# Kernel tuning notes

Hardware: AMD Instinct MI355X
Metric: run time of the kernel (lower is better)

Reference implementation:

```python
import jax, jax.numpy as jnp
import numpy as np

C = 256
RED = 8
DQK = C // RED  # 32


def setup_inputs() -> dict:
    key = jax.random.key(0)
    ks = jax.random.split(key, 8)
    B, H, W = 8, 64, 64
    x = jax.random.normal(ks[0], (B, C, H, W), dtype=jnp.float32)
    # 1x1 conv weights stored as [out, in]; biases [out]
    Wq = jax.random.normal(ks[1], (DQK, C), dtype=jnp.float32) * 0.02
    bq = jax.random.normal(ks[2], (DQK,), dtype=jnp.float32) * 0.02
    Wk = jax.random.normal(ks[3], (DQK, C), dtype=jnp.float32) * 0.02
    bk = jax.random.normal(ks[4], (DQK,), dtype=jnp.float32) * 0.02
    Wv = jax.random.normal(ks[5], (C, C), dtype=jnp.float32) * 0.02
    bv = jax.random.normal(ks[6], (C,), dtype=jnp.float32) * 0.02
    gamma = jax.random.normal(ks[7], (1,), dtype=jnp.float32) * 0.1
    return {"x": x, "Wq": Wq, "bq": bq, "Wk": Wk, "bk": bk, "Wv": Wv, "bv": bv, "gamma": gamma}


def reference(x, Wq, bq, Wk, bk, Wv, bv, gamma):
    B, Cc, H, W = x.shape
    N = H * W
    xf = x.reshape(B, Cc, N)                       # (B, C, N)
    # 1x1 convs == per-pixel dense projections
    q = jnp.einsum('dc,bcn->bdn', Wq, xf) + bq[None, :, None]   # (B, d, N)
    k = jnp.einsum('dc,bcn->bdn', Wk, xf) + bk[None, :, None]   # (B, d, N)
    v = jnp.einsum('ec,bcn->ben', Wv, xf) + bv[None, :, None]   # (B, C, N)
    # energy[b,i,j] = q[b,:,i] . k[b,:,j]; softmax over j (no scaling, SAGAN-style)
    energy = jnp.einsum('bdi,bdj->bij', q, k)      # (B, N, N)
    attn = jax.nn.softmax(energy, axis=-1)
    # out[b,c,i] = sum_j v[b,c,j] * attn[b,i,j]
    out = jnp.einsum('bcj,bij->bci', v, attn)      # (B, C, N)
    out = out.reshape(B, Cc, H, W)
    return gamma[0] * out + x
```

## Files before the change

### kernel.cpp

```cpp
#include <hip/hip_runtime.h>

#define NB 8
#define CCH 256
#define DQK 32
#define NPIX 4096

typedef __attribute__((ext_vector_type(8))) short short8;
typedef __attribute__((ext_vector_type(4))) float f32x4;
typedef __attribute__((ext_vector_type(4))) unsigned short ushort4v;

static __device__ __forceinline__ unsigned short f2bf(float f) {
  unsigned int u = __builtin_bit_cast(unsigned int, f);
  u += 0x7FFFu + ((u >> 16) & 1u);
  return (unsigned short)(u >> 16);
}
static __device__ __forceinline__ unsigned int pack2bf(float a, float b) {
  return (unsigned int)f2bf(a) | ((unsigned int)f2bf(b) << 16);
}

__global__ __launch_bounds__(256) void wconv_kernel(
    const float* __restrict__ Wq, const float* __restrict__ Wk,
    const float* __restrict__ Wv, unsigned short* __restrict__ Wbf) {
  const int e = (blockIdx.x * 256 + threadIdx.x) * 4;
  const int m = e >> 8, c = e & 255;
  const float* src;
  if (m < 32) src = Wq + (size_t)m * CCH;
  else if (m < 64) src = Wk + (size_t)(m - 32) * CCH;
  else src = Wv + (size_t)(m - 64) * CCH;
  const float4 v = *(const float4*)(src + c);
  ushort4v o;
  o[0] = f2bf(v.x); o[1] = f2bf(v.y); o[2] = f2bf(v.z); o[3] = f2bf(v.w);
  *(ushort4v*)(Wbf + e) = o;
}

__global__ __launch_bounds__(256) void proj_kernel(
    const float* __restrict__ x, const unsigned short* __restrict__ Wbf,
    const float* __restrict__ bq, const float* __restrict__ bk,
    const float* __restrict__ bv,
    unsigned short* __restrict__ Qb, unsigned short* __restrict__ Kb,
    unsigned short* __restrict__ Vb) {
  __shared__ unsigned short xs[32 * 256];
  const int t = threadIdx.x;
  const int b = blockIdx.x & 7;
  const int i0 = (blockIdx.x >> 3) * 32;
  const float* xb = x + (size_t)b * CCH * NPIX + i0;
  {
    const int ii = (t & 7) * 4;
    const int cb = t >> 3;
    const int sw8 = ((ii >> 2) & 7) << 3;
#pragma unroll
    for (int rep = 0; rep < 8; ++rep) {
      const int c = cb + 32 * rep;
      const float4 v = *(const float4*)(xb + (size_t)c * NPIX + ii);
      const float vv[4] = {v.x, v.y, v.z, v.w};
#pragma unroll
      for (int d = 0; d < 4; ++d) {
        const int cc = (c ^ sw8) ^ ((d & 1) << 4);
        xs[(ii + d) * 256 + cc] = f2bf(vv[d]);
      }
    }
  }
  __syncthreads();
  const int w = t >> 6, l = t & 63;
  const int lc = l & 15, lg = l >> 4;
  const int m0w = 80 * w;
  f32x4 acc[5][2];
#pragma unroll
  for (int mt = 0; mt < 5; ++mt)
#pragma unroll
    for (int nt = 0; nt < 2; ++nt) acc[mt][nt] = (f32x4){0.f, 0.f, 0.f, 0.f};

#pragma unroll
  for (int kk = 0; kk < 8; ++kk) {
    short8 af[5];
#pragma unroll
    for (int mt = 0; mt < 5; ++mt)
      af[mt] = *(const short8*)(Wbf + (size_t)(m0w + mt * 16 + lc) * CCH + kk * 32 + lg * 8);
#pragma unroll
    for (int nt = 0; nt < 2; ++nt) {
      const int i = nt * 16 + lc;
      const int s = (4 * nt + (lc >> 2)) & 7;
      const int cc = ((kk * 32 + lg * 8) ^ (s << 3)) ^ ((lc & 1) << 4);
      const short8 bfv = *(const short8*)&xs[i * 256 + cc];
#pragma unroll
      for (int mt = 0; mt < 5; ++mt)
        acc[mt][nt] = __builtin_amdgcn_mfma_f32_16x16x32_bf16(af[mt], bfv, acc[mt][nt], 0, 0, 0);
    }
  }
#pragma unroll
  for (int mt = 0; mt < 5; ++mt) {
    const int mbase = m0w + mt * 16;
    const int mrow = mbase + 4 * lg;
    if (mbase < 64) {
      const float* bias = (mbase < 32) ? (bq + mrow) : (bk + (mrow - 32));
      unsigned short* dst = (mbase < 32) ? (Qb + (size_t)b * NPIX * DQK + mrow)
                                         : (Kb + (size_t)b * NPIX * DQK + (mrow - 32));
      const float b0 = bias[0], b1 = bias[1], b2 = bias[2], b3 = bias[3];
#pragma unroll
      for (int nt = 0; nt < 2; ++nt) {
        const int i = i0 + nt * 16 + lc;
        ushort4v o;
        o[0] = f2bf(acc[mt][nt][0] + b0);
        o[1] = f2bf(acc[mt][nt][1] + b1);
        o[2] = f2bf(acc[mt][nt][2] + b2);
        o[3] = f2bf(acc[mt][nt][3] + b3);
        *(ushort4v*)(dst + (size_t)i * DQK) = o;
      }
    } else {
      const int vrow = mbase - 64 + 4 * lg;
#pragma unroll
      for (int jj = 0; jj < 4; ++jj) {
        const float bias = bv[vrow + jj];
        unsigned short* vdst = Vb + ((size_t)b * CCH + vrow + jj) * NPIX + i0;
#pragma unroll
        for (int nt = 0; nt < 2; ++nt)
          vdst[nt * 16 + lc] = f2bf(acc[mt][nt][jj] + bias);
      }
    }
  }
}

union AttnSmem {
  unsigned short p[2][64 * 64];
  float tsc[4][16 * 68];
};

__global__ __launch_bounds__(256, 2) void attn_kernel(
    const unsigned short* __restrict__ Qb,
    const unsigned short* __restrict__ Kb,
    const unsigned short* __restrict__ Vb,
    const float* __restrict__ x,
    const float* __restrict__ gammap,
    float* __restrict__ out) {
  __shared__ AttnSmem sm;
  __shared__ float l_lds[64];
  const int t = threadIdx.x;
  const int w = t >> 6, l = t & 63;
  const int lc = l & 15, lg = l >> 4;
  const int b = blockIdx.x & 7;
  const int q0 = (blockIdx.x >> 3) * 64;

  const unsigned short* Kl = Kb + (size_t)b * NPIX * DQK + (size_t)lc * DQK + lg * 8;
  const unsigned short* Vl = Vb + ((size_t)b * CCH + 64 * w + lc) * NPIX + lg * 8;
  const short8 qa = *(const short8*)(Qb + (size_t)b * NPIX * DQK +
                                     (size_t)(q0 + 16 * w + lc) * DQK + lg * 8);
  const f32x4 zero4 = {0.f, 0.f, 0.f, 0.f};
  const int pwb = (16 * w + lc) * 128;
  const int psw = (lc & 7) << 3;

  f32x4 acc[4][4];
#pragma unroll
  for (int mt = 0; mt < 4; ++mt)
#pragma unroll
    for (int ct = 0; ct < 4; ++ct) acc[mt][ct] = (f32x4){0.f, 0.f, 0.f, 0.f};
  float psum = 0.f;

  short8 vfA[8], vfB[8], kfA[4], kfB[4];

#pragma unroll
  for (int kt = 0; kt < 4; ++kt)
    kfA[kt] = *(const short8*)(Kl + (size_t)(kt * 16) * DQK);
#pragma unroll
  for (int kt = 0; kt < 4; ++kt) {
    const f32x4 s = __builtin_amdgcn_mfma_f32_16x16x32_bf16(kfA[kt], qa, zero4, 0, 0, 0);
    const float p0 = __expf(s[0]), p1 = __expf(s[1]);
    const float p2 = __expf(s[2]), p3 = __expf(s[3]);
    psum += (p0 + p1) + (p2 + p3);
    uint2 wv; wv.x = pack2bf(p0, p1); wv.y = pack2bf(p2, p3);
    *(uint2*)((char*)sm.p[0] + pwb + (((16 * kt + 4 * lg) ^ psw) << 1)) = wv;
  }
#pragma unroll
  for (int ct = 0; ct < 4; ++ct) {
    vfA[ct] = *(const short8*)(Vl + (size_t)(16 * ct) * NPIX);
    vfA[4 + ct] = *(const short8*)(Vl + (size_t)(16 * ct) * NPIX + 32);
  }
#pragma unroll
  for (int kt = 0; kt < 4; ++kt)
    kfB[kt] = *(const short8*)(Kl + (size_t)(64 + kt * 16) * DQK);
  __syncthreads();

#define ATTN_ITER(T, BUF, VF, KF_CUR, VF_NXT, KF_NXT)                               \
  {                                                                                 \
    const int t_ = (T);                                                             \
    if (t_ < 63) {                                                                  \
      const size_t kb2 = (size_t)(t_ + 1) * 64;                                     \
      _Pragma("unroll") for (int ct = 0; ct < 4; ++ct) {                            \
        VF_NXT[ct] = *(const short8*)(Vl + (size_t)(16 * ct) * NPIX + kb2);         \
        VF_NXT[4 + ct] = *(const short8*)(Vl + (size_t)(16 * ct) * NPIX + kb2 + 32);\
      }                                                                             \
      if (t_ < 62) {                                                                \
        const size_t kk2 = (size_t)(t_ + 2) * 64;                                   \
        _Pragma("unroll") for (int kt = 0; kt < 4; ++kt)                            \
          KF_NXT[kt] = *(const short8*)(Kl + (kk2 + kt * 16) * DQK);                \
      }                                                                             \
    }                                                                               \
    unsigned short* pb_ = sm.p[BUF];                                                \
    unsigned short* pb2_ = sm.p[(BUF) ^ 1];                                         \
    _Pragma("unroll") for (int ks2 = 0; ks2 < 2; ++ks2) {                           \
      short8 pa[4];                                                                 \
      _Pragma("unroll") for (int mt = 0; mt < 4; ++mt)                              \
        pa[mt] = *(const short8*)((const char*)pb_ + (16 * mt + lc) * 128 +         \
                                  (((32 * ks2 + 8 * lg) ^ psw) << 1));              \
      _Pragma("unroll") for (int ct = 0; ct < 4; ++ct)                              \
        _Pragma("unroll") for (int mt = 0; mt < 4; ++mt)                            \
          acc[mt][ct] = __builtin_amdgcn_mfma_f32_16x16x32_bf16(                    \
              pa[mt], VF[ks2 * 4 + ct], acc[mt][ct], 0, 0, 0);                      \
    }                                                                               \
    if (t_ < 63) {                                                                  \
      _Pragma("unroll") for (int kt = 0; kt < 4; ++kt) {                            \
        const f32x4 s = __builtin_amdgcn_mfma_f32_16x16x32_bf16(                    \
            KF_CUR[kt], qa, zero4, 0, 0, 0);                                        \
        const float p0 = __expf(s[0]), p1 = __expf(s[1]);                           \
        const float p2 = __expf(s[2]), p3 = __expf(s[3]);                           \
        psum += (p0 + p1) + (p2 + p3);                                              \
        uint2 wv; wv.x = pack2bf(p0, p1); wv.y = pack2bf(p2, p3);                   \
        *(uint2*)((char*)pb2_ + pwb + (((16 * kt + 4 * lg) ^ psw) << 1)) = wv;      \
      }                                                                             \
    }                                                                               \
    __syncthreads();                                                                \
  }

  for (int ks = 0; ks < 64; ks += 2) {
    ATTN_ITER(ks, 0, vfA, kfB, vfB, kfA);
    ATTN_ITER(ks + 1, 1, vfB, kfA, vfA, kfB);
  }
#undef ATTN_ITER

  {
    float v = psum;
    v += __shfl_xor(v, 16);
    v += __shfl_xor(v, 32);
    if (l < 16) l_lds[16 * w + lc] = v;
  }
  __syncthreads();

  const float g = gammap[0];
  float linv4[4][4];
#pragma unroll
  for (int mt = 0; mt < 4; ++mt)
#pragma unroll
    for (int jj = 0; jj < 4; ++jj)
      linv4[mt][jj] = 1.0f / l_lds[16 * mt + 4 * lg + jj];

  float* tw = sm.tsc[w];
  const float* xbp = x + (size_t)b * CCH * NPIX;
  float* ob = out + (size_t)b * CCH * NPIX;
#pragma unroll
  for (int ct = 0; ct < 4; ++ct) {
#pragma unroll
    for (int mt = 0; mt < 4; ++mt) {
      f32x4 o;
#pragma unroll
      for (int jj = 0; jj < 4; ++jj) o[jj] = g * acc[mt][ct][jj] * linv4[mt][jj];
      *(f32x4*)(tw + lc * 68 + 16 * mt + 4 * lg) = o;
    }
#pragma unroll
    for (int r = 0; r < 4; ++r) {
      const int crow = 4 * r + lg;
      const f32x4 o = *(const f32x4*)(tw + crow * 68 + lc * 4);
      const size_t idx = (size_t)(64 * w + 16 * ct + crow) * NPIX + (size_t)(q0 + lc * 4);
      const float4 xv = *(const float4*)(xbp + idx);
      float4 ov;
      ov.x = o[0] + xv.x; ov.y = o[1] + xv.y; ov.z = o[2] + xv.z; ov.w = o[3] + xv.w;
      *(float4*)(ob + idx) = ov;
    }
  }
}

extern "C" void kernel_launch(void* const* d_in, const int* in_sizes, int n_in,
                              void* d_out, int out_size, void* d_ws, size_t ws_size,
                              hipStream_t stream) {
  (void)in_sizes; (void)n_in; (void)out_size; (void)ws_size;
  const float* x     = (const float*)d_in[0];
  const float* Wq    = (const float*)d_in[1];
  const float* bq    = (const float*)d_in[2];
  const float* Wk    = (const float*)d_in[3];
  const float* bk    = (const float*)d_in[4];
  const float* Wv    = (const float*)d_in[5];
  const float* bv    = (const float*)d_in[6];
  const float* gamma = (const float*)d_in[7];

  unsigned short* Wbf = (unsigned short*)d_ws;
  unsigned short* Qb  = Wbf + 320 * CCH;
  unsigned short* Kb  = Qb + (size_t)NB * NPIX * DQK;
  unsigned short* Vb  = Kb + (size_t)NB * NPIX * DQK;

  wconv_kernel<<<80, 256, 0, stream>>>(Wq, Wk, Wv, Wbf);
  proj_kernel<<<1024, 256, 0, stream>>>(x, Wbf, bq, bk, bv, Qb, Kb, Vb);
  attn_kernel<<<512, 256, 0, stream>>>(Qb, Kb, Vb, x, gamma, (float*)d_out);
}
```

Measured before the change: 272.9 us.

## Pre-transpose x to bf16, fold log2e into Q, use exp2, lighter barrier

Adds a separate kernel that transposes x to pixel-major bf16, staged in the output buffer as scratch. The projection kernel then reads B fragments straight from global memory instead of through an LDS transpose, and each block covers 64 pixels instead of 32. Q is pre-scaled by log2(e) so attention can call exp2 directly, gamma is folded into the reciprocal row sum, and __syncthreads in the main loop becomes a raw waitcnt plus s_barrier. The extra kernel launch and the round trip of transposed x through global memory may cost more than the projection gains, and the attention loop dominates the runtime anyway.

```diff
diff --git a/kernel.cpp b/kernel.cpp
--- a/kernel.cpp
+++ b/kernel.cpp
@@ -33,77 +33,80 @@
   *(ushort4v*)(Wbf + e) = o;
 }
 
+__global__ __launch_bounds__(256) void xt_kernel(
+    const float* __restrict__ x, unsigned short* __restrict__ xT) {
+  const int t = threadIdx.x;
+  const int b = blockIdx.x & 7;
+  const int p = (blockIdx.x >> 3) * 64 + (t & 63);
+  const int w = t >> 6;
+  const float* xb = x + (size_t)b * CCH * NPIX + p;
+  unsigned short* dst = xT + ((size_t)b * NPIX + p) * CCH + 64 * w;
+#pragma unroll
+  for (int g = 0; g < 8; ++g) {
+    short8 o;
+#pragma unroll
+    for (int j = 0; j < 8; ++j)
+      o[j] = (short)f2bf(xb[(size_t)(64 * w + 8 * g + j) * NPIX]);
+    *(short8*)(dst + 8 * g) = o;
+  }
+}
+
 __global__ __launch_bounds__(256) void proj_kernel(
-    const float* __restrict__ x, const unsigned short* __restrict__ Wbf,
+    const unsigned short* __restrict__ xT, const unsigned short* __restrict__ Wbf,
     const float* __restrict__ bq, const float* __restrict__ bk,
     const float* __restrict__ bv,
     unsigned short* __restrict__ Qb, unsigned short* __restrict__ Kb,
     unsigned short* __restrict__ Vb) {
-  __shared__ unsigned short xs[32 * 256];
   const int t = threadIdx.x;
   const int b = blockIdx.x & 7;
-  const int i0 = (blockIdx.x >> 3) * 32;
-  const float* xb = x + (size_t)b * CCH * NPIX + i0;
-  {
-    const int ii = (t & 7) * 4;
-    const int cb = t >> 3;
-    const int sw8 = ((ii >> 2) & 7) << 3;
-#pragma unroll
-    for (int rep = 0; rep < 8; ++rep) {
-      const int c = cb + 32 * rep;
-      const float4 v = *(const float4*)(xb + (size_t)c * NPIX + ii);
-      const float vv[4] = {v.x, v.y, v.z, v.w};
-#pragma unroll
-      for (int d = 0; d < 4; ++d) {
-        const int cc = (c ^ sw8) ^ ((d & 1) << 4);
-        xs[(ii + d) * 256 + cc] = f2bf(vv[d]);
-      }
-    }
-  }
-  __syncthreads();
+  const int i0 = (blockIdx.x >> 3) * 64;
   const int w = t >> 6, l = t & 63;
   const int lc = l & 15, lg = l >> 4;
   const int m0w = 80 * w;
-  f32x4 acc[5][2];
+  const unsigned short* xrow = xT + ((size_t)b * NPIX + i0 + lc) * CCH + lg * 8;
+  const unsigned short* wrow = Wbf + (size_t)(m0w + lc) * CCH + lg * 8;
+
+  f32x4 acc[5][4];
 #pragma unroll
   for (int mt = 0; mt < 5; ++mt)
 #pragma unroll
-    for (int nt = 0; nt < 2; ++nt) acc[mt][nt] = (f32x4){0.f, 0.f, 0.f, 0.f};
+    for (int nt = 0; nt < 4; ++nt) acc[mt][nt] = (f32x4){0.f, 0.f, 0.f, 0.f};
 
 #pragma unroll
   for (int kk = 0; kk < 8; ++kk) {
     short8 af[5];
 #pragma unroll
     for (int mt = 0; mt < 5; ++mt)
-      af[mt] = *(const short8*)(Wbf + (size_t)(m0w + mt * 16 + lc) * CCH + kk * 32 + lg * 8);
-#pragma unroll
-    for (int nt = 0; nt < 2; ++nt) {
-      const int i = nt * 16 + lc;
-      const int s = (4 * nt + (lc >> 2)) & 7;
-      const int cc = ((kk * 32 + lg * 8) ^ (s << 3)) ^ ((lc & 1) << 4);
-      const short8 bfv = *(const short8*)&xs[i * 256 + cc];
+      af[mt] = *(const short8*)(wrow + (size_t)(mt * 16) * CCH + kk * 32);
+    short8 bf[4];
+#pragma unroll
+    for (int nt = 0; nt < 4; ++nt)
+      bf[nt] = *(const short8*)(xrow + (size_t)(nt * 16) * CCH + kk * 32);
+#pragma unroll
+    for (int nt = 0; nt < 4; ++nt)
 #pragma unroll
       for (int mt = 0; mt < 5; ++mt)
-        acc[mt][nt] = __builtin_amdgcn_mfma_f32_16x16x32_bf16(af[mt], bfv, acc[mt][nt], 0, 0, 0);
-    }
+        acc[mt][nt] = __builtin_amdgcn_mfma_f32_16x16x32_bf16(af[mt], bf[nt], acc[mt][nt], 0, 0, 0);
   }
 #pragma unroll
   for (int mt = 0; mt < 5; ++mt) {
     const int mbase = m0w + mt * 16;
     const int mrow = mbase + 4 * lg;
     if (mbase < 64) {
-      const float* bias = (mbase < 32) ? (bq + mrow) : (bk + (mrow - 32));
-      unsigned short* dst = (mbase < 32) ? (Qb + (size_t)b * NPIX * DQK + mrow)
-                                         : (Kb + (size_t)b * NPIX * DQK + (mrow - 32));
+      const bool isQ = (mbase < 32);
+      const float scale = isQ ? 1.44269504f : 1.0f;
+      const float* bias = isQ ? (bq + mrow) : (bk + (mrow - 32));
+      unsigned short* dst = isQ ? (Qb + (size_t)b * NPIX * DQK + mrow)
+                                : (Kb + (size_t)b * NPIX * DQK + (mrow - 32));
       const float b0 = bias[0], b1 = bias[1], b2 = bias[2], b3 = bias[3];
 #pragma unroll
-      for (int nt = 0; nt < 2; ++nt) {
+      for (int nt = 0; nt < 4; ++nt) {
         const int i = i0 + nt * 16 + lc;
         ushort4v o;
-        o[0] = f2bf(acc[mt][nt][0] + b0);
-        o[1] = f2bf(acc[mt][nt][1] + b1);
-        o[2] = f2bf(acc[mt][nt][2] + b2);
-        o[3] = f2bf(acc[mt][nt][3] + b3);
+        o[0] = f2bf((acc[mt][nt][0] + b0) * scale);
+        o[1] = f2bf((acc[mt][nt][1] + b1) * scale);
+        o[2] = f2bf((acc[mt][nt][2] + b2) * scale);
+        o[3] = f2bf((acc[mt][nt][3] + b3) * scale);
         *(ushort4v*)(dst + (size_t)i * DQK) = o;
       }
     } else {
@@ -113,7 +116,7 @@
         const float bias = bv[vrow + jj];
         unsigned short* vdst = Vb + ((size_t)b * CCH + vrow + jj) * NPIX + i0;
 #pragma unroll
-        for (int nt = 0; nt < 2; ++nt)
+        for (int nt = 0; nt < 4; ++nt)
           vdst[nt * 16 + lc] = f2bf(acc[mt][nt][jj] + bias);
       }
     }
@@ -163,8 +166,8 @@
 #pragma unroll
   for (int kt = 0; kt < 4; ++kt) {
     const f32x4 s = __builtin_amdgcn_mfma_f32_16x16x32_bf16(kfA[kt], qa, zero4, 0, 0, 0);
-    const float p0 = __expf(s[0]), p1 = __expf(s[1]);
-    const float p2 = __expf(s[2]), p3 = __expf(s[3]);
+    const float p0 = __builtin_exp2f(s[0]), p1 = __builtin_exp2f(s[1]);
+    const float p2 = __builtin_exp2f(s[2]), p3 = __builtin_exp2f(s[3]);
     psum += (p0 + p1) + (p2 + p3);
     uint2 wv; wv.x = pack2bf(p0, p1); wv.y = pack2bf(p2, p3);
     *(uint2*)((char*)sm.p[0] + pwb + (((16 * kt + 4 * lg) ^ psw) << 1)) = wv;
@@ -182,7 +185,7 @@
 #define ATTN_ITER(T, BUF, VF, KF_CUR, VF_NXT, KF_NXT)                               \
   {                                                                                 \
     const int t_ = (T);                                                             \
-    if (t_ < 63) {                                                                  \
+    if (t_ < 63) {      \
       const size_t kb2 = (size_t)(t_ + 1) * 64;                                     \
       _Pragma("unroll") for (int ct = 0; ct < 4; ++ct) {                            \
         VF_NXT[ct] = *(const short8*)(Vl + (size_t)(16 * ct) * NPIX + kb2);         \
@@ -210,14 +213,14 @@
       _Pragma("unroll") for (int kt = 0; kt < 4; ++kt) {                            \
         const f32x4 s = __builtin_amdgcn_mfma_f32_16x16x32_bf16(                    \
             KF_CUR[kt], qa, zero4, 0, 0, 0);                                        \
-        const float p0 = __expf(s[0]), p1 = __expf(s[1]);                           \
-        const float p2 = __expf(s[2]), p3 = __expf(s[3]);                           \
+        const float p0 = __builtin_exp2f(s[0]), p1 = __builtin_exp2f(s[1]);         \
+        const float p2 = __builtin_exp2f(s[2]), p3 = __builtin_exp2f(s[3]);         \
         psum += (p0 + p1) + (p2 + p3);                                              \
         uint2 wv; wv.x = pack2bf(p0, p1); wv.y = pack2bf(p2, p3);                   \
         *(uint2*)((char*)pb2_ + pwb + (((16 * kt + 4 * lg) ^ psw) << 1)) = wv;      \
       }                                                                             \
     }                                                                               \
-    __syncthreads();                                                                \
+    asm volatile("s_waitcnt lgkmcnt(0)\n\ts_barrier" ::: "memory");                 \
   }
 
   for (int ks = 0; ks < 64; ks += 2) {
@@ -240,7 +243,7 @@
   for (int mt = 0; mt < 4; ++mt)
 #pragma unroll
     for (int jj = 0; jj < 4; ++jj)
-      linv4[mt][jj] = 1.0f / l_lds[16 * mt + 4 * lg + jj];
+      linv4[mt][jj] = g / l_lds[16 * mt + 4 * lg + jj];
 
   float* tw = sm.tsc[w];
   const float* xbp = x + (size_t)b * CCH * NPIX;
@@ -251,7 +254,7 @@
     for (int mt = 0; mt < 4; ++mt) {
       f32x4 o;
 #pragma unroll
-      for (int jj = 0; jj < 4; ++jj) o[jj] = g * acc[mt][ct][jj] * linv4[mt][jj];
+      for (int jj = 0; jj < 4; ++jj) o[jj] = acc[mt][ct][jj] * linv4[mt][jj];
       *(f32x4*)(tw + lc * 68 + 16 * mt + 4 * lg) = o;
     }
 #pragma unroll
@@ -284,8 +287,10 @@
   unsigned short* Qb  = Wbf + 320 * CCH;
   unsigned short* Kb  = Qb + (size_t)NB * NPIX * DQK;
   unsigned short* Vb  = Kb + (size_t)NB * NPIX * DQK;
+  unsigned short* xT  = (unsigned short*)d_out;
 
   wconv_kernel<<<80, 256, 0, stream>>>(Wq, Wk, Wv, Wbf);
-  proj_kernel<<<1024, 256, 0, stream>>>(x, Wbf, bq, bk, bv, Qb, Kb, Vb);
+  xt_kernel<<<512, 256, 0, stream>>>(x, xT);
+  proj_kernel<<<512, 256, 0, stream>>>(xT, Wbf, bq, bk, bv, Qb, Kb, Vb);
   attn_kernel<<<512, 256, 0, stream>>>(Qb, Kb, Vb, x, gamma, (float*)d_out);
 }
```

New measurement: 289.0 us. 1.06x slower.
